# Performance work log

Hardware: AMD Instinct MI355X
Metric: run time of the kernel (lower is better)

Reference implementation:

```python
import jax, jax.numpy as jnp
import numpy as np

TOKENS, IN_F, OUT_F = 8192, 4096, 4096

def setup_inputs() -> dict:
    key = jax.random.key(0)
    k1, k2, k3, k4 = jax.random.split(key, 4)
    # int8 activations and weights in [-127, 127]
    x = jax.random.randint(k1, (TOKENS, IN_F), -127, 128, dtype=jnp.int32).astype(jnp.int8)
    weight = jax.random.randint(k2, (OUT_F, IN_F), -127, 128, dtype=jnp.int32).astype(jnp.int8)  # [out, in]
    # static per-output-channel dequant scale (fp16), small so fp16 output doesn't overflow
    dequant_scale = (jax.random.uniform(k3, (OUT_F,), dtype=jnp.float32) * 1e-3).astype(jnp.float16)
    bias = (jax.random.normal(k4, (OUT_F,), dtype=jnp.float32)).astype(jnp.float16)
    return {"x": x, "weight": weight, "dequant_scale": dequant_scale, "bias": bias}

def reference(x, weight, dequant_scale, bias):
    # int8 GEMM with int32 accumulation: [tokens, in] @ [in, out] -> [tokens, out]
    acc = jax.lax.dot_general(
        x, weight.T,
        dimension_numbers=(((1,), (0,)), ((), ())),
        preferred_element_type=jnp.int32,
    )
    # static per-output-channel dequant, cast to fp16, add fp16 bias
    out = (acc.astype(jnp.float32) * dequant_scale.astype(jnp.float32)[None, :]).astype(jnp.float16)
    out = out + bias[None, :]
    # module returns (output, output_bias)
    return (out, bias)
```

## Files before the change

### kernel.cpp

```cpp
#include <hip/hip_runtime.h>
#include <hip/hip_fp16.h>
#include <stdint.h>

typedef __attribute__((ext_vector_type(4))) int int32x4;
typedef __attribute__((ext_vector_type(4))) float float32x4;

#define TOKENS 8192
#define IN_F   4096
#define OUT_F  4096
#define BM 256
#define BN 256
#define BK 128
#define NT (IN_F / BK)
#define ESTR 260

__global__ __launch_bounds__(256)
void pack_all_kernel(const int* __restrict__ x32, const int* __restrict__ w32,
                     const float* __restrict__ bias,
                     uint32_t* __restrict__ x8, uint32_t* __restrict__ w8,
                     float* __restrict__ bias_out)
{
    const int gid = blockIdx.x * 256 + threadIdx.x;
    if (gid < OUT_F / 4)
        ((float32x4*)bias_out)[gid] = ((const float32x4*)bias)[gid];

    const int nx4 = TOKENS * IN_F / 4;
    const int nw4 = OUT_F * IN_F / 4;
    for (int i = gid; i < nx4 + nw4; i += gridDim.x * 256) {
        const int* s; uint32_t* d; int j;
        if (i < nx4) { s = x32; d = x8; j = i; }
        else         { s = w32; d = w8; j = i - nx4; }
        int32x4 v = ((const int32x4*)s)[j];
        d[j] = (uint32_t)(v[0] & 0xff) | ((uint32_t)(v[1] & 0xff) << 8) |
               ((uint32_t)(v[2] & 0xff) << 16) | ((uint32_t)v[3] << 24);
    }
}

__global__ __launch_bounds__(512, 2)
void w8a8_gemm_kernel(const int8_t* __restrict__ x,
                      const int8_t* __restrict__ w,
                      const float* __restrict__ scale,
                      const float* __restrict__ bias,
                      float* __restrict__ out)
{
    __shared__ int8_t smem[131072];
    int8_t* lA = smem;
    int8_t* lB = smem + 65536;

    const int tid = threadIdx.x;
    const int wv  = tid >> 6;
    const int l   = tid & 63;
    const int wqm = wv >> 1;
    const int wqn = wv & 1;

    const int bn = blockIdx.x;
    const int bm = blockIdx.y;

    const int8_t* baseA = x + (size_t)bm * BM * IN_F;
    const int8_t* baseB = w + (size_t)bn * BN * IN_F;

    const int seg0 = wv * 2, seg1 = wv * 2 + 1;
    const int r8   = l >> 3;
    const int swc  = (((l & 7) ^ r8) << 4);

    const int fr  = l & 15;
    const int xk  = (l & 7) << 4;
    const int cb0 = (l >> 4) << 4;

    int32x4 acc[2][2][2][4];
#pragma unroll
    for (int a0 = 0; a0 < 2; ++a0)
#pragma unroll
        for (int a1 = 0; a1 < 2; ++a1)
#pragma unroll
            for (int a2 = 0; a2 < 2; ++a2)
#pragma unroll
                for (int a3 = 0; a3 < 4; ++a3)
                    acc[a0][a1][a2][a3] = (int32x4){0, 0, 0, 0};

    int32x4 aF[2][2];
    int32x4 bF0[4][2];
    int32x4 bF1[4][2];

    auto stage_half = [&](int h4) {
        const int kt_ = h4 >> 2;
        const int wh_ = h4 & 3;
        const int8_t* sb = (wh_ < 2) ? baseA : baseB;
        int8_t* db = ((wh_ < 2) ? lA : lB) + ((kt_ & 1) << 15) + ((wh_ & 1) << 14);
        const size_t co = (size_t)kt_ * BK + swc;
        const size_t rb = (size_t)((wh_ & 1) * 128 + r8);
        __builtin_amdgcn_global_load_lds(
            (const __attribute__((address_space(1))) void*)(sb + (rb + seg0 * 8) * IN_F + co),
            (__attribute__((address_space(3))) void*)(db + seg0 * 1024), 16, 0, 0);
        __builtin_amdgcn_global_load_lds(
            (const __attribute__((address_space(1))) void*)(sb + (rb + seg1 * 8) * IN_F + co),
            (__attribute__((address_space(3))) void*)(db + seg1 * 1024), 16, 0, 0);
    };

#define LDA(MH)                                                                        \
    do {                                                                               \
        _Pragma("unroll") for (int mi = 0; mi < 2; ++mi)                               \
        _Pragma("unroll") for (int ks = 0; ks < 2; ++ks)                               \
            aF[mi][ks] = *(const int32x4*)&lAb[((MH) << 14) +                          \
                (wqm * 32 + mi * 16 + fr) * 128 + (((ks * 64) + cb0) ^ xk)];           \
    } while (0)

#define LDB(NH, DST)                                                                   \
    do {                                                                               \
        _Pragma("unroll") for (int ni = 0; ni < 4; ++ni)                               \
        _Pragma("unroll") for (int ks = 0; ks < 2; ++ks)                               \
            DST[ni][ks] = *(const int32x4*)&lBb[((NH) << 14) +                         \
                (wqn * 64 + ni * 16 + fr) * 128 + (((ks * 64) + cb0) ^ xk)];           \
    } while (0)

#define MMAQ(MH, NH, BF)                                                               \
    do {                                                                               \
        _Pragma("unroll") for (int mi = 0; mi < 2; ++mi)                               \
        _Pragma("unroll") for (int ni = 0; ni < 4; ++ni)                               \
        _Pragma("unroll") for (int ks = 0; ks < 2; ++ks)                               \
            acc[MH][NH][mi][ni] = __builtin_amdgcn_mfma_i32_16x16x64_i8(               \
                aF[mi][ks], BF[ni][ks], acc[MH][NH][mi][ni], 0, 0, 0);                 \
    } while (0)

#define PH(MH, NH, BF)                                                                 \
    do {                                                                               \
        __builtin_amdgcn_s_barrier();                                                  \
        asm volatile("s_waitcnt lgkmcnt(0)" ::: "memory");                             \
        __builtin_amdgcn_s_setprio(1);                                                 \
        MMAQ(MH, NH, BF);                                                              \
        __builtin_amdgcn_s_setprio(0);                                                 \
        __builtin_amdgcn_s_barrier();                                                  \
    } while (0)

    stage_half(0); stage_half(3); stage_half(1); stage_half(2);
    stage_half(4); stage_half(7);
    asm volatile("s_waitcnt vmcnt(4)" ::: "memory");
    __builtin_amdgcn_s_barrier();

    for (int t = 0; t < NT; ++t) {
        const int8_t* lAb = lA + ((t & 1) << 15);
        const int8_t* lBb = lB + ((t & 1) << 15);

        LDA(0); LDB(0, bF0);
        if (t + 1 < NT) stage_half(4 * (t + 1) + 1);
        PH(0, 0, bF0);

        LDB(1, bF1);
        if (t + 1 < NT) stage_half(4 * (t + 1) + 2);
        PH(0, 1, bF1);

        LDA(1);
        if (t + 2 < NT) stage_half(4 * (t + 2) + 0);
        PH(1, 1, bF1);

        if (t + 2 < NT) stage_half(4 * (t + 2) + 3);
        if (t + 2 < NT)      asm volatile("s_waitcnt vmcnt(4)" ::: "memory");
        else if (t + 1 < NT) asm volatile("s_waitcnt vmcnt(0)" ::: "memory");
        PH(1, 0, bF0);
    }

    __syncthreads();
    int* eL = (int*)smem;
    const int c4   = tid & 63;
    const int rowt = tid >> 6;
    const float32x4 sc4 = ((const float32x4*)scale)[bn * 64 + c4];
    const float32x4 bf4 = ((const float32x4*)bias )[bn * 64 + c4];
    const __half bh[4] = { __float2half(bf4[0]), __float2half(bf4[1]),
                           __float2half(bf4[2]), __float2half(bf4[3]) };
    const int r0 = (l >> 4) << 2;
    const int wr0 = (wqm & 1) * 32 + r0;

    for (int c = 0; c < 4; ++c) {
        if ((wqm >> 1) == (c & 1)) {
            const int MH = c >> 1;
#pragma unroll
            for (int NH = 0; NH < 2; ++NH)
#pragma unroll
                for (int mi = 0; mi < 2; ++mi)
#pragma unroll
                    for (int ni = 0; ni < 4; ++ni)
#pragma unroll
                        for (int r = 0; r < 4; ++r)
                            eL[(wr0 + mi * 16 + r) * ESTR +
                               NH * 128 + wqn * 64 + ni * 16 + fr] = acc[MH][NH][mi][ni][r];
        }
        __syncthreads();
#pragma unroll
        for (int p = 0; p < 8; ++p) {
            const int rl = p * 8 + rowt;
            int32x4 v = *(const int32x4*)&eL[rl * ESTR + c4 * 4];
            float32x4 o;
#pragma unroll
            for (int j = 0; j < 4; ++j) {
                __half h = __float2half((float)v[j] * sc4[j]);
                o[j] = __half2float(__hadd(h, bh[j]));
            }
            const size_t rowg = (size_t)(bm * 256 + c * 64 + rl);
            ((float32x4*)out)[rowg * (OUT_F / 4) + bn * 64 + c4] = o;
        }
        __syncthreads();
    }
#undef LDA
#undef LDB
#undef MMAQ
#undef PH
}

extern "C" void kernel_launch(void* const* d_in, const int* in_sizes, int n_in,
                              void* d_out, int out_size, void* d_ws, size_t ws_size,
                              hipStream_t stream)
{
    const int*   x32   = (const int*)d_in[0];
    const int*   w32   = (const int*)d_in[1];
    const float* scale = (const float*)d_in[2];
    const float* bias  = (const float*)d_in[3];
    float* out = (float*)d_out;

    int8_t* x8 = (int8_t*)d_ws;
    int8_t* w8 = x8 + (size_t)TOKENS * IN_F;

    pack_all_kernel<<<3072, 256, 0, stream>>>(x32, w32, bias, (uint32_t*)x8, (uint32_t*)w8,
                                              out + (size_t)TOKENS * OUT_F);

    dim3 grid(OUT_F / BN, TOKENS / BM);
    w8a8_gemm_kernel<<<grid, 512, 0, stream>>>(x8, w8, scale, bias, out);
}
```

Before: 196.3 us.

## Merge four MFMA phases per K-tile into two and hoist load addresses

```diff
diff --git a/kernel.cpp b/kernel.cpp
--- a/kernel.cpp
+++ b/kernel.cpp
@@ -63,6 +63,11 @@
     const int r8   = l >> 3;
     const int swc  = (((l & 7) ^ r8) << 4);
 
+    const int8_t* pA0 = baseA + (size_t)(seg0 * 8 + r8) * IN_F + swc;
+    const int8_t* pA1 = baseA + (size_t)(seg1 * 8 + r8) * IN_F + swc;
+    const int8_t* pB0 = baseB + (size_t)(seg0 * 8 + r8) * IN_F + swc;
+    const int8_t* pB1 = baseB + (size_t)(seg1 * 8 + r8) * IN_F + swc;
+
     const int fr  = l & 15;
     const int xk  = (l & 7) << 4;
     const int cb0 = (l >> 4) << 4;
@@ -85,15 +90,15 @@
     auto stage_half = [&](int h4) {
         const int kt_ = h4 >> 2;
         const int wh_ = h4 & 3;
-        const int8_t* sb = (wh_ < 2) ? baseA : baseB;
+        const size_t off = (size_t)(wh_ & 1) * (128 * IN_F) + (size_t)kt_ * BK;
+        const int8_t* s0 = ((wh_ < 2) ? pA0 : pB0) + off;
+        const int8_t* s1 = ((wh_ < 2) ? pA1 : pB1) + off;
         int8_t* db = ((wh_ < 2) ? lA : lB) + ((kt_ & 1) << 15) + ((wh_ & 1) << 14);
-        const size_t co = (size_t)kt_ * BK + swc;
-        const size_t rb = (size_t)((wh_ & 1) * 128 + r8);
         __builtin_amdgcn_global_load_lds(
-            (const __attribute__((address_space(1))) void*)(sb + (rb + seg0 * 8) * IN_F + co),
+            (const __attribute__((address_space(1))) void*)s0,
             (__attribute__((address_space(3))) void*)(db + seg0 * 1024), 16, 0, 0);
         __builtin_amdgcn_global_load_lds(
-            (const __attribute__((address_space(1))) void*)(sb + (rb + seg1 * 8) * IN_F + co),
+            (const __attribute__((address_space(1))) void*)s1,
             (__attribute__((address_space(3))) void*)(db + seg1 * 1024), 16, 0, 0);
     };
 
@@ -122,41 +127,38 @@
                 aF[mi][ks], BF[ni][ks], acc[MH][NH][mi][ni], 0, 0, 0);                 \
     } while (0)
 
-#define PH(MH, NH, BF)                                                                 \
-    do {                                                                               \
-        __builtin_amdgcn_s_barrier();                                                  \
-        asm volatile("s_waitcnt lgkmcnt(0)" ::: "memory");                             \
-        __builtin_amdgcn_s_setprio(1);                                                 \
-        MMAQ(MH, NH, BF);                                                              \
-        __builtin_amdgcn_s_setprio(0);                                                 \
-        __builtin_amdgcn_s_barrier();                                                  \
-    } while (0)
-
-    stage_half(0); stage_half(3); stage_half(1); stage_half(2);
-    stage_half(4); stage_half(7);
-    asm volatile("s_waitcnt vmcnt(4)" ::: "memory");
+    stage_half(0); stage_half(1); stage_half(2); stage_half(3);
+    stage_half(4);
+    asm volatile("s_waitcnt vmcnt(2)" ::: "memory");
     __builtin_amdgcn_s_barrier();
 
     for (int t = 0; t < NT; ++t) {
         const int8_t* lAb = lA + ((t & 1) << 15);
         const int8_t* lBb = lB + ((t & 1) << 15);
 
-        LDA(0); LDB(0, bF0);
-        if (t + 1 < NT) stage_half(4 * (t + 1) + 1);
-        PH(0, 0, bF0);
-
-        LDB(1, bF1);
-        if (t + 1 < NT) stage_half(4 * (t + 1) + 2);
-        PH(0, 1, bF1);
+        LDA(0); LDB(0, bF0); LDB(1, bF1);
+        if (t + 1 < NT) {
+            stage_half(4 * (t + 1) + 1);
+            stage_half(4 * (t + 1) + 2);
+            stage_half(4 * (t + 1) + 3);
+        }
+        __builtin_amdgcn_s_barrier();
+        asm volatile("s_waitcnt lgkmcnt(0)" ::: "memory");
+        __builtin_amdgcn_s_setprio(1);
+        MMAQ(0, 0, bF0); MMAQ(0, 1, bF1);
+        __builtin_amdgcn_s_setprio(0);
+        __builtin_amdgcn_s_barrier();
 
         LDA(1);
         if (t + 2 < NT) stage_half(4 * (t + 2) + 0);
-        PH(1, 1, bF1);
-
-        if (t + 2 < NT) stage_half(4 * (t + 2) + 3);
-        if (t + 2 < NT)      asm volatile("s_waitcnt vmcnt(4)" ::: "memory");
+        if (t + 2 < NT)      asm volatile("s_waitcnt vmcnt(2)" ::: "memory");
         else if (t + 1 < NT) asm volatile("s_waitcnt vmcnt(0)" ::: "memory");
-        PH(1, 0, bF0);
+        __builtin_amdgcn_s_barrier();
+        asm volatile("s_waitcnt lgkmcnt(0)" ::: "memory");
+        __builtin_amdgcn_s_setprio(1);
+        MMAQ(1, 0, bF0); MMAQ(1, 1, bF1);
+        __builtin_amdgcn_s_setprio(0);
+        __builtin_amdgcn_s_barrier();
     }
 
     __syncthreads();
@@ -203,7 +205,6 @@
 #undef LDA
 #undef LDB
 #undef MMAQ
-#undef PH
 }
 
 extern "C" void kernel_launch(void* const* d_in, const int* in_sizes, int n_in,
```

After: 196.5 us. About the same (+0.1%).
